# Kernel tuning notes

Hardware: AMD Instinct MI355X
Metric: run time of the kernel (lower is better)

Reference implementation:

```python
import jax, jax.numpy as jnp
import numpy as np

N_NODES = 20000


def _segment_softmax(alpha, dst, num_nodes):
    # numerically-stable softmax over edges grouped by destination node
    m = jax.ops.segment_max(alpha, dst, num_segments=num_nodes)
    m = jnp.where(jnp.isfinite(m), m, 0.0)
    a = jnp.exp(alpha - m[dst])
    denom = jax.ops.segment_sum(a, dst, num_segments=num_nodes)
    return a / denom[dst]


def mgcn_conv(x, src, dst, edge_type, basis, att, weight, root, bias, num_nodes):
    # x: [N, in], basis: [B, in, out], att: [R, B], weight: [R, out=in]
    x_i = x[dst]                                   # [E, in] target feats
    x_j = x[src]                                   # [E, in] source feats
    # per-edge attention logit: sum_d x_i[d] * w_r[d] * x_j[d]
    alpha = jnp.sum(x_i * weight[edge_type] * x_j, axis=1)   # [E]
    alpha = _segment_softmax(alpha, dst, num_nodes)          # [E]
    # basis-decomposed per-edge transform: x_j @ (att_r . basis)
    t = jnp.einsum('ei,bio->ebo', x_j, basis)                # [E, B, out]
    msg = jnp.einsum('ebo,eb->eo', t, att[edge_type])        # [E, out]
    msg = msg * alpha[:, None]
    out = jax.ops.segment_sum(msg, dst, num_segments=num_nodes)  # [N, out]
    return out + x @ root + bias


def setup_inputs() -> dict:
    key = jax.random.key(0)
    ks = jax.random.split(key, 16)
    E, D, R, B, N = 32768, 128, 474, 64, N_NODES
    s = 0.05
    return {
        'entity': jnp.arange(N, dtype=jnp.int64) if jax.config.jax_enable_x64 else jnp.arange(N, dtype=jnp.int32),
        'edge_index': jax.random.randint(ks[0], (2, E), 0, N, dtype=jnp.int32),
        'edge_type': jax.random.randint(ks[1], (E,), 0, R, dtype=jnp.int32),
        'emb_table': jax.random.normal(ks[2], (N, D), dtype=jnp.float32),
        'basis1': jax.random.normal(ks[3], (B, D, D), dtype=jnp.float32) * s,
        'att1': jax.random.normal(ks[4], (R, B), dtype=jnp.float32) * s,
        'weight1': jax.random.normal(ks[5], (R, D), dtype=jnp.float32) * s,
        'root1': jax.random.normal(ks[6], (D, D), dtype=jnp.float32) * s,
        'bias1': jnp.zeros((D,), dtype=jnp.float32),
        'basis2': jax.random.normal(ks[7], (B, D, D), dtype=jnp.float32) * s,
        'att2': jax.random.normal(ks[8], (R, B), dtype=jnp.float32) * s,
        'weight2': jax.random.normal(ks[9], (R, D), dtype=jnp.float32) * s,
        'root2': jax.random.normal(ks[10], (D, D), dtype=jnp.float32) * s,
        'bias2': jnp.zeros((D,), dtype=jnp.float32),
    }


def reference(entity, edge_index, edge_type, emb_table,
              basis1, att1, weight1, root1, bias1,
              basis2, att2, weight2, root2, bias2):
    src, dst = edge_index[0], edge_index[1]   # PyG: (source j, target i)
    x = emb_table[entity]                     # embedding lookup
    h = jax.nn.relu(mgcn_conv(x, src, dst, edge_type, basis1, att1,
                              weight1, root1, bias1, N_NODES))
    # dropout is identity at inference
    out = mgcn_conv(h, src, dst, edge_type, basis2, att2,
                    weight2, root2, bias2, N_NODES)
    return out
```

## Files before the change

kernel.cpp:

```cpp
#include <hip/hip_runtime.h>
#include <hip/hip_bf16.h>

#define N_NODES 20000
#define N_EDGES 32768
#define DIM 128
#define N_REL 474
#define N_BASIS 64
#define TILE_E 64
#define MAXCH (N_EDGES / TILE_E + N_REL)
#define WSTRIDE 260
#define HIST_BLKS 16
#define EDGES_PER_HIST (N_EDGES / HIST_BLKS)
#define LOGIT_BLKS (N_EDGES / 4)
#define ROOT_BLKS ((N_NODES + 63) / 64)

typedef __bf16 bf16x8 __attribute__((ext_vector_type(8)));
typedef float f32x4 __attribute__((ext_vector_type(4)));

__device__ __forceinline__ unsigned short f2b(float f) {
    unsigned u = __float_as_uint(f);
    unsigned r = (u + 0x7FFFu + ((u >> 16) & 1u)) >> 16;
    return (unsigned short)r;
}
__device__ __forceinline__ float b2f(unsigned short s) {
    return __uint_as_float(((unsigned)s) << 16);
}
__device__ __forceinline__ __bf16 u2b(unsigned short u) {
    union { unsigned short u; __bf16 b; } c; c.u = u; return c.b;
}
__device__ __forceinline__ int4 packrelu8(float4 a0, float4 a1) {
    int4 v;
    v.x = (int)((unsigned)f2b(fmaxf(a0.x, 0.f)) | ((unsigned)f2b(fmaxf(a0.y, 0.f)) << 16));
    v.y = (int)((unsigned)f2b(fmaxf(a0.z, 0.f)) | ((unsigned)f2b(fmaxf(a0.w, 0.f)) << 16));
    v.z = (int)((unsigned)f2b(fmaxf(a1.x, 0.f)) | ((unsigned)f2b(fmaxf(a1.y, 0.f)) << 16));
    v.w = (int)((unsigned)f2b(fmaxf(a1.z, 0.f)) | ((unsigned)f2b(fmaxf(a1.w, 0.f)) << 16));
    return v;
}

__global__ __launch_bounds__(256) void prepmix_kernel(const float4* __restrict__ emb,
                                                      const int* __restrict__ entity,
                                                      const int* __restrict__ etype,
                                                      ushort4* __restrict__ xb4,
                                                      float4* __restrict__ zreg, int zcount4,
                                                      int* __restrict__ partial,
                                                      const float* __restrict__ att1,
                                                      const float* __restrict__ basis1,
                                                      unsigned short* __restrict__ W1,
                                                      const float* __restrict__ att2,
                                                      const float* __restrict__ basis2,
                                                      unsigned short* __restrict__ W2) {
    __shared__ __align__(16) unsigned short bt[64 * WSTRIDE];
    int t = threadIdx.x;
    if (blockIdx.x < 1024) {
        int wi = blockIdx.x;
        const float* att   = (wi >= 512) ? att2 : att1;
        const float* basis = (wi >= 512) ? basis2 : basis1;
        unsigned short* W  = (wi >= 512) ? W2 : W1;
        int io0 = (wi & 63) * 256;
        int r0 = ((wi >> 6) & 7) * 64;
#pragma unroll
        for (int p = 0; p < 16; p++) {
            int c = t + 256 * p;
            int k = c >> 6, of = c & 63;
            float4 v = *(const float4*)(basis + (size_t)k * (DIM * DIM) + io0 + of * 4);
            ushort4 s;
            s.x = f2b(v.x); s.y = f2b(v.y); s.z = f2b(v.z); s.w = f2b(v.w);
            *(ushort4*)&bt[k * WSTRIDE + of * 4] = s;
        }
        __syncthreads();

        int w = t >> 6, l = t & 63, n = l & 15, q = l >> 4;
        f32x4 acc[4][4] = {};
#pragma unroll
        for (int kb = 0; kb < 2; kb++) {
            int kbase = kb * 32 + q * 8;
            bf16x8 a[4];
#pragma unroll
            for (int rt = 0; rt < 4; rt++) {
                int rm = min(r0 + rt * 16 + n, N_REL - 1);
                const float* ap = att + (size_t)rm * N_BASIS + kbase;
#pragma unroll
                for (int j = 0; j < 8; j++) a[rt][j] = u2b(f2b(ap[j]));
            }
#pragma unroll
            for (int c = 0; c < 4; c++) {
                int ob = w * 64 + c * 16 + n;
                bf16x8 b;
#pragma unroll
                for (int j = 0; j < 8; j++) b[j] = u2b(bt[(kbase + j) * WSTRIDE + ob]);
#pragma unroll
                for (int rt = 0; rt < 4; rt++)
                    acc[rt][c] = __builtin_amdgcn_mfma_f32_16x16x32_bf16(a[rt], b, acc[rt][c], 0, 0, 0);
            }
        }
#pragma unroll
        for (int rt = 0; rt < 4; rt++) {
#pragma unroll
            for (int c = 0; c < 4; c++) {
                int col = io0 + w * 64 + c * 16 + n;
#pragma unroll
                for (int rg = 0; rg < 4; rg++) {
                    int r = r0 + rt * 16 + q * 4 + rg;
                    if (r < N_REL) W[(size_t)r * (DIM * DIM) + col] = f2b(acc[rt][c][rg]);
                }
            }
        }
    } else {
        int pb = blockIdx.x - 1024;
        int gtid = pb * 256 + t;
        int gsz = 1024 * 256;
        int total4 = N_NODES * DIM / 4;
        for (int i = gtid; i < total4; i += gsz) {
            int n = i >> 5, rem = i & 31;
            float4 v = emb[(size_t)entity[n] * 32 + rem];
            ushort4 s;
            s.x = f2b(v.x); s.y = f2b(v.y); s.z = f2b(v.z); s.w = f2b(v.w);
            xb4[i] = s;
        }
        float4 z = make_float4(0.f, 0.f, 0.f, 0.f);
        for (int i = gtid; i < zcount4; i += gsz) zreg[i] = z;
        if (pb < HIST_BLKS) {
            int* ih = (int*)bt;
            for (int i = t; i < N_REL; i += 256) ih[i] = 0;
            __syncthreads();
            int e0 = pb * EDGES_PER_HIST;
            for (int e = e0 + t; e < e0 + EDGES_PER_HIST; e += 256)
                atomicAdd(&ih[etype[e]], 1);
            __syncthreads();
            for (int i = t; i < N_REL; i += 256) partial[pb * N_REL + i] = ih[i];
        }
    }
}

__global__ void scanr_kernel(const int* __restrict__ partial, int* __restrict__ offs,
                             int* __restrict__ cursor, int* __restrict__ chunk_r,
                             int* __restrict__ chunk_o, int* __restrict__ nchunks) {
    __shared__ int s[512];
    __shared__ int lnc;
    int t = threadIdx.x;
    int v = 0;
    if (t < N_REL) {
#pragma unroll
        for (int k = 0; k < HIST_BLKS; k++) v += partial[k * N_REL + t];
    }
    s[t] = v;
    if (t == 0) lnc = 0;
    __syncthreads();
    for (int d = 1; d < 512; d <<= 1) {
        int add = (t >= d) ? s[t - d] : 0;
        __syncthreads();
        s[t] += add;
        __syncthreads();
    }
    int excl = s[t] - v;
    if (t < N_REL) { offs[t] = excl; cursor[t] = excl; }
    if (t == 0) offs[N_REL] = N_EDGES;
    if (t < N_REL && v > 0) {
        int nc = (v + TILE_E - 1) / TILE_E;
        int cb = atomicAdd(&lnc, nc);
        for (int c = 0; c < nc; c++) { chunk_r[cb + c] = t; chunk_o[cb + c] = excl + c * TILE_E; }
    }
    __syncthreads();
    if (t == 0) *nchunks = lnc;
}

__global__ __launch_bounds__(256) void fused_kernel(const unsigned short* __restrict__ xb,
                                                    const float* __restrict__ xf,
                                                    const float* __restrict__ w,
                                                    const int* __restrict__ src,
                                                    const int* __restrict__ dst,
                                                    const int* __restrict__ et,
                                                    int* __restrict__ cursor,
                                                    int* __restrict__ eids,
                                                    int do_scatter,
                                                    float* __restrict__ alpha,
                                                    float* __restrict__ den,
                                                    const float* __restrict__ rootM,
                                                    const float* __restrict__ bias,
                                                    float* __restrict__ target) {
    __shared__ __align__(16) unsigned short xrf[8192];
    int t = threadIdx.x;
    if (blockIdx.x < LOGIT_BLKS) {
        int wid = (blockIdx.x * 256 + t) >> 6;
        int lane = t & 63;
        int s = src[wid], d = dst[wid], r = et[wid];
        if (do_scatter && lane == 0) {
            int p = atomicAdd(&cursor[r], 1);
            eids[p] = wid;
        }
        float2 wv = ((const float2*)(w + (size_t)r * DIM))[lane];
        float v;
        if (xf == nullptr) {
            unsigned ax = ((const unsigned*)(xb + (size_t)s * DIM))[lane];
            unsigned bx = ((const unsigned*)(xb + (size_t)d * DIM))[lane];
            v = b2f((unsigned short)(ax & 0xFFFF)) * wv.x * b2f((unsigned short)(bx & 0xFFFF))
              + b2f((unsigned short)(ax >> 16)) * wv.y * b2f((unsigned short)(bx >> 16));
        } else {
            float2 axf = ((const float2*)(xf + (size_t)s * DIM))[lane];
            float2 bxf = ((const float2*)(xf + (size_t)d * DIM))[lane];
            v = fmaxf(axf.x, 0.f) * wv.x * fmaxf(bxf.x, 0.f)
              + fmaxf(axf.y, 0.f) * wv.y * fmaxf(bxf.y, 0.f);
        }
        for (int off = 32; off > 0; off >>= 1) v += __shfl_xor(v, off, 64);
        if (lane == 0) {
            float a = expf(v);
            alpha[wid] = a;
            atomicAdd(&den[d], a);
        }
    } else {
        int n0 = (blockIdx.x - LOGIT_BLKS) * 64;
#pragma unroll
        for (int p = 0; p < 4; p++) {
            int c = t + 256 * p;
            int g = c >> 6;
            int rt = g >> 2, kb = g & 3;
            int q = (c >> 4) & 3, m = c & 15;
            int row = n0 + rt * 16 + m;
            int oct = kb * 4 + q;
            int4 v = make_int4(0, 0, 0, 0);
            if (row < N_NODES) {
                if (xf == nullptr) {
                    v = *(const int4*)(xb + (size_t)row * DIM + oct * 8);
                } else {
                    const float4* sp = (const float4*)(xf + (size_t)row * DIM + oct * 8);
                    v = packrelu8(sp[0], sp[1]);
                }
            }
            *(int4*)&xrf[c * 8] = v;
        }
        __syncthreads();

        int w_ = t >> 6, l = t & 63, n = l & 15, q = l >> 4;
        f32x4 acc[2][4] = {};
#pragma unroll
        for (int kb = 0; kb < 4; kb++) {
            bf16x8 a[4];
#pragma unroll
            for (int rt = 0; rt < 4; rt++) a[rt] = *(const bf16x8*)&xrf[((rt * 4 + kb) * 64 + l) * 8];
            int kbase = kb * 32 + q * 8;
#pragma unroll
            for (int c = 0; c < 2; c++) {
                int col = (w_ * 2 + c) * 16 + n;
                bf16x8 b;
#pragma unroll
                for (int j = 0; j < 8; j++) b[j] = u2b(f2b(rootM[(kbase + j) * DIM + col]));
#pragma unroll
                for (int rt = 0; rt < 4; rt++)
                    acc[c][rt] = __builtin_amdgcn_mfma_f32_16x16x32_bf16(a[rt], b, acc[c][rt], 0, 0, 0);
            }
        }
#pragma unroll
        for (int c = 0; c < 2; c++) {
            int col = (w_ * 2 + c) * 16 + n;
            float bo = bias[col];
#pragma unroll
            for (int rt = 0; rt < 4; rt++) {
#pragma unroll
                for (int rg = 0; rg < 4; rg++) {
                    int row = n0 + rt * 16 + q * 4 + rg;
                    if (row < N_NODES)
                        target[(size_t)row * DIM + col] = acc[c][rt][rg] + bo;
                }
            }
        }
    }
}

__global__ __launch_bounds__(256) void msg_kernel(const unsigned short* __restrict__ xb,
                                                  const float* __restrict__ xf,
                                                  const unsigned short* __restrict__ W,
                                                  const int* __restrict__ chunk_r,
                                                  const int* __restrict__ chunk_off,
                                                  const int* __restrict__ nchunks,
                                                  const int* __restrict__ eids,
                                                  const int* __restrict__ offs,
                                                  const int* __restrict__ src,
                                                  const int* __restrict__ dst,
                                                  const float* __restrict__ ae,
                                                  const float* __restrict__ denom,
                                                  float* __restrict__ outacc) {
    if ((int)blockIdx.x >= *nchunks) return;
    int r = chunk_r[blockIdx.x];
    int base = chunk_off[blockIdx.x];
    int nE = min(TILE_E, offs[r + 1] - base);
    const unsigned short* Wr = W + (size_t)r * (DIM * DIM);

    __shared__ unsigned short wt[128 * 136];
    __shared__ unsigned short xjf[8192];
    __shared__ float scf[TILE_E];
    __shared__ int sdd[TILE_E];

    int t = threadIdx.x;
    if (t < TILE_E) {
        if (t < nE) {
            int e = eids[base + t];
            int d_ = dst[e];
            sdd[t] = d_;
            scf[t] = ae[e] / denom[d_];
        } else { sdd[t] = 0; scf[t] = 0.f; }
    }
#pragma unroll
    for (int p = 0; p < 4; p++) {
        int c = t + 256 * p;
        int g = c >> 6;
        int rt = g >> 2, kb = g & 3;
        int q = (c >> 4) & 3, m = c & 15;
        int e = rt * 16 + m;
        int oct = kb * 4 + q;
        int4 v = make_int4(0, 0, 0, 0);
        if (e < nE) {
            size_t rowoff = (size_t)src[eids[base + e]] * DIM + oct * 8;
            if (xf == nullptr) {
                v = *(const int4*)(xb + rowoff);
            } else {
                const float4* sp = (const float4*)(xf + rowoff);
                v = packrelu8(sp[0], sp[1]);
            }
        }
        *(int4*)&xjf[c * 8] = v;
    }
#pragma unroll
    for (int p = 0; p < 8; p++) {
        int c = t + 256 * p;
        int k = c >> 4, oct = c & 15;
        int4 v = *(const int4*)(Wr + k * DIM + oct * 8);
        *(int4*)&wt[k * 136 + oct * 8] = v;
    }
    __syncthreads();

    int w = t >> 6, l = t & 63, n = l & 15, q = l >> 4;
    f32x4 acc[2][4] = {};
#pragma unroll
    for (int kb = 0; kb < 4; kb++) {
        bf16x8 a[4];
#pragma unroll
        for (int rt = 0; rt < 4; rt++) a[rt] = *(const bf16x8*)&xjf[((rt * 4 + kb) * 64 + l) * 8];
        int kbase = kb * 32 + q * 8;
#pragma unroll
        for (int c = 0; c < 2; c++) {
            int ob = (w * 2 + c) * 16 + n;
            bf16x8 b;
#pragma unroll
            for (int j = 0; j < 8; j++) b[j] = u2b(wt[(kbase + j) * 136 + ob]);
#pragma unroll
            for (int rt = 0; rt < 4; rt++)
                acc[c][rt] = __builtin_amdgcn_mfma_f32_16x16x32_bf16(a[rt], b, acc[c][rt], 0, 0, 0);
        }
    }
#pragma unroll
    for (int c = 0; c < 2; c++) {
        int col = (w * 2 + c) * 16 + n;
#pragma unroll
        for (int rt = 0; rt < 4; rt++) {
#pragma unroll
            for (int rg = 0; rg < 4; rg++) {
                int e = rt * 16 + q * 4 + rg;
                if (e < nE)
                    atomicAdd(&outacc[(size_t)sdd[e] * DIM + col], scf[e] * acc[c][rt][rg]);
            }
        }
    }
}

extern "C" void kernel_launch(void* const* d_in, const int* in_sizes, int n_in,
                              void* d_out, int out_size, void* d_ws, size_t ws_size,
                              hipStream_t stream) {
    const int N = N_NODES, E = N_EDGES, R = N_REL;

    const int* entity = (const int*)d_in[0];
    const int* eidx   = (const int*)d_in[1];
    const int* src    = eidx;
    const int* dst    = eidx + E;
    const int* etype  = (const int*)d_in[2];
    const float* emb  = (const float*)d_in[3];
    const float* basis1 = (const float*)d_in[4];
    const float* att1   = (const float*)d_in[5];
    const float* w1     = (const float*)d_in[6];
    const float* root1  = (const float*)d_in[7];
    const float* bias1  = (const float*)d_in[8];
    const float* basis2 = (const float*)d_in[9];
    const float* att2   = (const float*)d_in[10];
    const float* w2     = (const float*)d_in[11];
    const float* root2  = (const float*)d_in[12];
    const float* bias2  = (const float*)d_in[13];
    float* out = (float*)d_out;

    size_t off = 0;
    auto alloc = [&](size_t bytes) -> void* {
        void* p = (char*)d_ws + off;
        off += (bytes + 255) & ~(size_t)255;
        return p;
    };
    unsigned short* W1 = (unsigned short*)alloc((size_t)R * DIM * DIM * 2);
    unsigned short* W2 = (unsigned short*)alloc((size_t)R * DIM * DIM * 2);
    unsigned short* xb = (unsigned short*)alloc((size_t)N * DIM * 2);
    float* acc1   = (float*)alloc((size_t)N * DIM * 4);
    float* zreg   = (float*)alloc((size_t)2 * N * 4);
    float* denom1 = zreg;
    float* denom2 = zreg + N;
    float* alpha  = (float*)alloc((size_t)E * 4);
    int* partial  = (int*)alloc((size_t)HIST_BLKS * R * 4);
    int* nchunks  = (int*)alloc(256);
    int* offs     = (int*)alloc((size_t)(R + 1) * 4);
    int* cursor   = (int*)alloc((size_t)R * 4);
    int* eids     = (int*)alloc((size_t)E * 4);
    int* chunk_r  = (int*)alloc((size_t)MAXCH * 4);
    int* chunk_o  = (int*)alloc((size_t)MAXCH * 4);

    int zcount4 = 2 * N / 4;

    prepmix_kernel<<<2048, 256, 0, stream>>>((const float4*)emb, entity, etype,
                                             (ushort4*)xb, (float4*)zreg, zcount4, partial,
                                             att1, basis1, W1, att2, basis2, W2);
    scanr_kernel<<<1, 512, 0, stream>>>(partial, offs, cursor, chunk_r, chunk_o, nchunks);

    fused_kernel<<<LOGIT_BLKS + ROOT_BLKS, 256, 0, stream>>>(
        xb, nullptr, w1, src, dst, etype, cursor, eids, 1, alpha, denom1, root1, bias1, acc1);
    msg_kernel<<<MAXCH, 256, 0, stream>>>(xb, nullptr, W1, chunk_r, chunk_o, nchunks,
                                          eids, offs, src, dst, alpha, denom1, acc1);

    fused_kernel<<<LOGIT_BLKS + ROOT_BLKS, 256, 0, stream>>>(
        nullptr, acc1, w2, src, dst, etype, cursor, eids, 0, alpha, denom2, root2, bias2, out);
    msg_kernel<<<MAXCH, 256, 0, stream>>>(nullptr, acc1, W2, chunk_r, chunk_o, nchunks,
                                          eids, offs, src, dst, alpha, denom2, out);
}
```

Baseline: 225.2 us.

## Reuse basis tiles across relation groups, swizzle LDS, and narrow logit lanes

The weight-mixing stage now uses 128 blocks, each looping over all eight relation groups, so every block converts and stages its basis slice in LDS once instead of eight times. The LDS layouts for the basis tile in prepmix and the weight tile in msg_kernel are XOR-swizzled to cut bank conflicts on the strided column reads feeding the MFMA. The logit computation assigns 16 lanes per edge with 128-bit vector loads and a shorter shuffle reduction, replacing 64 lanes per edge. The trade-off is less parallelism in the W-mix stage, whose blocks now run longer serial loops.

```diff
diff --git a/kernel.cpp b/kernel.cpp
--- a/kernel.cpp
+++ b/kernel.cpp
@@ -11,7 +11,8 @@
 #define WSTRIDE 260
 #define HIST_BLKS 16
 #define EDGES_PER_HIST (N_EDGES / HIST_BLKS)
-#define LOGIT_BLKS (N_EDGES / 4)
+#define WMIX_BLKS 128
+#define LOGIT_BLKS (N_EDGES / 16)
 #define ROOT_BLKS ((N_NODES + 63) / 64)
 
 typedef __bf16 bf16x8 __attribute__((ext_vector_type(8)));
@@ -35,6 +36,10 @@
     v.z = (int)((unsigned)f2b(fmaxf(a1.x, 0.f)) | ((unsigned)f2b(fmaxf(a1.y, 0.f)) << 16));
     v.w = (int)((unsigned)f2b(fmaxf(a1.z, 0.f)) | ((unsigned)f2b(fmaxf(a1.w, 0.f)) << 16));
     return v;
+}
+__device__ __forceinline__ float dot2bf(unsigned a, unsigned b, float wx, float wy) {
+    return b2f((unsigned short)(a & 0xFFFFu)) * wx * b2f((unsigned short)(b & 0xFFFFu))
+         + b2f((unsigned short)(a >> 16)) * wy * b2f((unsigned short)(b >> 16));
 }
 
 __global__ __launch_bounds__(256) void prepmix_kernel(const float4* __restrict__ emb,
@@ -51,13 +56,12 @@
                                                       unsigned short* __restrict__ W2) {
     __shared__ __align__(16) unsigned short bt[64 * WSTRIDE];
     int t = threadIdx.x;
-    if (blockIdx.x < 1024) {
+    if (blockIdx.x < WMIX_BLKS) {
         int wi = blockIdx.x;
-        const float* att   = (wi >= 512) ? att2 : att1;
-        const float* basis = (wi >= 512) ? basis2 : basis1;
-        unsigned short* W  = (wi >= 512) ? W2 : W1;
+        const float* att   = (wi >= 64) ? att2 : att1;
+        const float* basis = (wi >= 64) ? basis2 : basis1;
+        unsigned short* W  = (wi >= 64) ? W2 : W1;
         int io0 = (wi & 63) * 256;
-        int r0 = ((wi >> 6) & 7) * 64;
 #pragma unroll
         for (int p = 0; p < 16; p++) {
             int c = t + 256 * p;
@@ -65,48 +69,54 @@
             float4 v = *(const float4*)(basis + (size_t)k * (DIM * DIM) + io0 + of * 4);
             ushort4 s;
             s.x = f2b(v.x); s.y = f2b(v.y); s.z = f2b(v.z); s.w = f2b(v.w);
-            *(ushort4*)&bt[k * WSTRIDE + of * 4] = s;
+            int ofx = of ^ (((k >> 3) & 7) << 2);
+            *(ushort4*)&bt[k * WSTRIDE + ofx * 4] = s;
         }
         __syncthreads();
 
         int w = t >> 6, l = t & 63, n = l & 15, q = l >> 4;
-        f32x4 acc[4][4] = {};
-#pragma unroll
-        for (int kb = 0; kb < 2; kb++) {
-            int kbase = kb * 32 + q * 8;
-            bf16x8 a[4];
+#pragma unroll 1
+        for (int rg = 0; rg < 8; rg++) {
+            int r0 = rg * 64;
+            f32x4 acc[4][4] = {};
+#pragma unroll
+            for (int kb = 0; kb < 2; kb++) {
+                int kbase = kb * 32 + q * 8;
+                int sx = ((kb * 4 + q) & 7) << 4;
+                bf16x8 a[4];
+#pragma unroll
+                for (int rt = 0; rt < 4; rt++) {
+                    int rm = min(r0 + rt * 16 + n, N_REL - 1);
+                    const float* ap = att + (size_t)rm * N_BASIS + kbase;
+#pragma unroll
+                    for (int j = 0; j < 8; j++) a[rt][j] = u2b(f2b(ap[j]));
+                }
+#pragma unroll
+                for (int c = 0; c < 4; c++) {
+                    int ob = (w * 64 + c * 16 + n) ^ sx;
+                    bf16x8 b;
+#pragma unroll
+                    for (int j = 0; j < 8; j++) b[j] = u2b(bt[(kbase + j) * WSTRIDE + ob]);
+#pragma unroll
+                    for (int rt = 0; rt < 4; rt++)
+                        acc[rt][c] = __builtin_amdgcn_mfma_f32_16x16x32_bf16(a[rt], b, acc[rt][c], 0, 0, 0);
+                }
+            }
 #pragma unroll
             for (int rt = 0; rt < 4; rt++) {
-                int rm = min(r0 + rt * 16 + n, N_REL - 1);
-                const float* ap = att + (size_t)rm * N_BASIS + kbase;
-#pragma unroll
-                for (int j = 0; j < 8; j++) a[rt][j] = u2b(f2b(ap[j]));
-            }
-#pragma unroll
-            for (int c = 0; c < 4; c++) {
-                int ob = w * 64 + c * 16 + n;
-                bf16x8 b;
-#pragma unroll
-                for (int j = 0; j < 8; j++) b[j] = u2b(bt[(kbase + j) * WSTRIDE + ob]);
-#pragma unroll
-                for (int rt = 0; rt < 4; rt++)
-                    acc[rt][c] = __builtin_amdgcn_mfma_f32_16x16x32_bf16(a[rt], b, acc[rt][c], 0, 0, 0);
-            }
-        }
-#pragma unroll
-        for (int rt = 0; rt < 4; rt++) {
-#pragma unroll
-            for (int c = 0; c < 4; c++) {
-                int col = io0 + w * 64 + c * 16 + n;
-#pragma unroll
-                for (int rg = 0; rg < 4; rg++) {
-                    int r = r0 + rt * 16 + q * 4 + rg;
-                    if (r < N_REL) W[(size_t)r * (DIM * DIM) + col] = f2b(acc[rt][c][rg]);
+#pragma unroll
+                for (int c = 0; c < 4; c++) {
+                    int col = io0 + w * 64 + c * 16 + n;
+#pragma unroll
+                    for (int g = 0; g < 4; g++) {
+                        int r = r0 + rt * 16 + q * 4 + g;
+                        if (r < N_REL) W[(size_t)r * (DIM * DIM) + col] = f2b(acc[rt][c][g]);
+                    }
                 }
             }
         }
     } else {
-        int pb = blockIdx.x - 1024;
+        int pb = blockIdx.x - WMIX_BLKS;
         int gtid = pb * 256 + t;
         int gsz = 1024 * 256;
         int total4 = N_NODES * DIM / 4;
@@ -181,30 +191,44 @@
     __shared__ __align__(16) unsigned short xrf[8192];
     int t = threadIdx.x;
     if (blockIdx.x < LOGIT_BLKS) {
-        int wid = (blockIdx.x * 256 + t) >> 6;
-        int lane = t & 63;
-        int s = src[wid], d = dst[wid], r = et[wid];
+        int eg = blockIdx.x * 16 + (t >> 4);
+        int lane = t & 15;
+        int s = src[eg], d = dst[eg], r = et[eg];
         if (do_scatter && lane == 0) {
             int p = atomicAdd(&cursor[r], 1);
-            eids[p] = wid;
-        }
-        float2 wv = ((const float2*)(w + (size_t)r * DIM))[lane];
+            eids[p] = eg;
+        }
+        const float4* wp = (const float4*)(w + (size_t)r * DIM);
+        float4 w0 = wp[lane * 2], w1 = wp[lane * 2 + 1];
         float v;
         if (xf == nullptr) {
-            unsigned ax = ((const unsigned*)(xb + (size_t)s * DIM))[lane];
-            unsigned bx = ((const unsigned*)(xb + (size_t)d * DIM))[lane];
-            v = b2f((unsigned short)(ax & 0xFFFF)) * wv.x * b2f((unsigned short)(bx & 0xFFFF))
-              + b2f((unsigned short)(ax >> 16)) * wv.y * b2f((unsigned short)(bx >> 16));
+            int4 av = ((const int4*)(xb + (size_t)s * DIM))[lane];
+            int4 bv = ((const int4*)(xb + (size_t)d * DIM))[lane];
+            v = dot2bf((unsigned)av.x, (unsigned)bv.x, w0.x, w0.y)
+              + dot2bf((unsigned)av.y, (unsigned)bv.y, w0.z, w0.w)
+              + dot2bf((unsigned)av.z, (unsigned)bv.z, w1.x, w1.y)
+              + dot2bf((unsigned)av.w, (unsigned)bv.w, w1.z, w1.w);
         } else {
-            float2 axf = ((const float2*)(xf + (size_t)s * DIM))[lane];
-            float2 bxf = ((const float2*)(xf + (size_t)d * DIM))[lane];
-            v = fmaxf(axf.x, 0.f) * wv.x * fmaxf(bxf.x, 0.f)
-              + fmaxf(axf.y, 0.f) * wv.y * fmaxf(bxf.y, 0.f);
-        }
-        for (int off = 32; off > 0; off >>= 1) v += __shfl_xor(v, off, 64);
+            const float4* ap = (const float4*)(xf + (size_t)s * DIM);
+            const float4* bp = (const float4*)(xf + (size_t)d * DIM);
+            float4 a0 = ap[lane * 2], a1 = ap[lane * 2 + 1];
+            float4 b0 = bp[lane * 2], b1 = bp[lane * 2 + 1];
+            v = fmaxf(a0.x, 0.f) * w0.x * fmaxf(b0.x, 0.f)
+              + fmaxf(a0.y, 0.f) * w0.y * fmaxf(b0.y, 0.f)
+              + fmaxf(a0.z, 0.f) * w0.z * fmaxf(b0.z, 0.f)
+              + fmaxf(a0.w, 0.f) * w0.w * fmaxf(b0.w, 0.f)
+              + fmaxf(a1.x, 0.f) * w1.x * fmaxf(b1.x, 0.f)
+              + fmaxf(a1.y, 0.f) * w1.y * fmaxf(b1.y, 0.f)
+              + fmaxf(a1.z, 0.f) * w1.z * fmaxf(b1.z, 0.f)
+              + fmaxf(a1.w, 0.f) * w1.w * fmaxf(b1.w, 0.f);
+        }
+        v += __shfl_xor(v, 8, 64);
+        v += __shfl_xor(v, 4, 64);
+        v += __shfl_xor(v, 2, 64);
+        v += __shfl_xor(v, 1, 64);
         if (lane == 0) {
             float a = expf(v);
-            alpha[wid] = a;
+            alpha[eg] = a;
             atomicAdd(&den[d], a);
         }
     } else {
@@ -285,8 +309,8 @@
     int nE = min(TILE_E, offs[r + 1] - base);
     const unsigned short* Wr = W + (size_t)r * (DIM * DIM);
 
-    __shared__ unsigned short wt[128 * 136];
-    __shared__ unsigned short xjf[8192];
+    __shared__ __align__(16) unsigned short wt[128 * 136];
+    __shared__ __align__(16) unsigned short xjf[8192];
     __shared__ float scf[TILE_E];
     __shared__ int sdd[TILE_E];
 
@@ -324,7 +348,8 @@
         int c = t + 256 * p;
         int k = c >> 4, oct = c & 15;
         int4 v = *(const int4*)(Wr + k * DIM + oct * 8);
-        *(int4*)&wt[k * 136 + oct * 8] = v;
+        int oct2 = oct ^ (((k >> 3) & 7) << 1);
+        *(int4*)&wt[k * 136 + oct2 * 8] = v;
     }
     __syncthreads();
 
@@ -336,9 +361,10 @@
 #pragma unroll
         for (int rt = 0; rt < 4; rt++) a[rt] = *(const bf16x8*)&xjf[((rt * 4 + kb) * 64 + l) * 8];
         int kbase = kb * 32 + q * 8;
+        int sx = ((kb * 4 + q) & 7) << 4;
 #pragma unroll
         for (int c = 0; c < 2; c++) {
-            int ob = (w * 2 + c) * 16 + n;
+            int ob = ((w * 2 + c) * 16 + n) ^ sx;
             bf16x8 b;
 #pragma unroll
             for (int j = 0; j < 8; j++) b[j] = u2b(wt[(kbase + j) * 136 + ob]);
@@ -409,7 +435,7 @@
 
     int zcount4 = 2 * N / 4;
 
-    prepmix_kernel<<<2048, 256, 0, stream>>>((const float4*)emb, entity, etype,
+    prepmix_kernel<<<WMIX_BLKS + 1024, 256, 0, stream>>>((const float4*)emb, entity, etype,
                                              (ushort4*)xb, (float4*)zreg, zcount4, partial,
                                              att1, basis1, W1, att2, basis2, W2);
     scanr_kernel<<<1, 512, 0, stream>>>(partial, offs, cursor, chunk_r, chunk_o, nchunks);
```

Measured after the change: 219.7 us. -2.4%, faster.
